# Optimization experiments

Hardware: AMD Instinct MI355X
Metric: run time of the kernel (lower is better)

## Reference

```python
import jax, jax.numpy as jnp
import numpy as np

N, E, D_IN, D_OUT, K = 50000, 800000, 128, 128, 3

def setup_inputs() -> dict:
    key = jax.random.key(0)
    k1, k2, k3, k4, k5 = jax.random.split(key, 5)
    feat = jax.random.normal(k1, (N, D_IN), dtype=jnp.float32)
    src = jax.random.randint(k2, (E,), 0, N)
    dst = jax.random.randint(k3, (E,), 0, N)
    theta = 0.1 * jax.random.normal(k4, (K + 1,), dtype=jnp.float32)
    # xavier-uniform-like linear weight [out, in]
    lim = float(np.sqrt(6.0 / (D_IN + D_OUT)))
    W = jax.random.uniform(k5, (D_OUT, D_IN), minval=-lim, maxval=lim, dtype=jnp.float32)
    return {"feat": feat, "src": src, "dst": dst, "theta": theta, "W": W}

def reference(feat, src, dst, theta, W):
    n = feat.shape[0]
    # in-degree per destination node, clamped to >= 1
    deg = jax.ops.segment_sum(jnp.ones_like(dst, dtype=feat.dtype), dst, num_segments=n)
    d_invsqrt = jnp.maximum(deg, 1.0) ** -0.5  # [N]
    d_invsqrt = d_invsqrt[:, None]

    def L_prime(x):
        # -D^{-1/2} A D^{-1/2} x  (A aggregates src -> dst)
        msg = (x * d_invsqrt)[src]                      # [E, D]
        agg = jax.ops.segment_sum(msg, dst, num_segments=n)
        return -agg * d_invsqrt

    k = theta.shape[0] - 1
    h = theta[0] * feat
    T_km2 = feat
    T_km1 = L_prime(feat)
    if k >= 1:
        h = h + theta[1] * (T_km1 + 1.0) * 0.5
    for order in range(2, k + 1):
        T_k = 2.0 * L_prime(T_km1) - T_km2
        h = h + theta[order] * (T_k + 1.0) * 0.5
        T_km2, T_km1 = T_km1, T_k

    out = h @ W.T  # linear, no bias
    return jax.nn.leaky_relu(out, negative_slope=0.01)
```

## Files before the change

### kernel.cpp

```cpp
#include <hip/hip_runtime.h>

#define NN 50000
#define EE 800000
#define D 128
#define PARTSZ 6250

static inline size_t align_up(size_t x, size_t a) { return (x + a - 1) & ~(a - 1); }

__device__ __forceinline__ unsigned pack_bf16(float a, float b) {
    unsigned ua = __float_as_uint(a), ub = __float_as_uint(b);
    unsigned ra = (ua + 0x7fffu + ((ua >> 16) & 1u)) >> 16;
    unsigned rb = (ub + 0x7fffu + ((ub >> 16) & 1u)) & 0xffff0000u;
    return ra | rb;
}
__device__ __forceinline__ float bf_lo(unsigned u) { return __uint_as_float(u << 16); }
__device__ __forceinline__ float bf_hi(unsigned u) { return __uint_as_float(u & 0xffff0000u); }

__global__ void zero_kernel(int* __restrict__ p, int n) {
    int i = blockIdx.x * blockDim.x + threadIdx.x;
    if (i < n) p[i] = 0;
}

__global__ __launch_bounds__(256) void deg_kernel(const int* __restrict__ dst,
                                                  int* __restrict__ deg, int E) {
    int part = blockIdx.x & 7;
    int nch = gridDim.x >> 3;
    int chunk = blockIdx.x >> 3;
    int per = (E + nch - 1) / nch;
    int beg = chunk * per;
    int end = min(E, beg + per);
    int plo = part * PARTSZ, phi = plo + PARTSZ;
    for (int e = beg + threadIdx.x; e < end; e += 256) {
        int d = dst[e];
        if (d >= plo && d < phi) atomicAdd(&deg[d], 1);
    }
}

__global__ void dinv_kernel(const int* __restrict__ deg, float* __restrict__ dinv,
                            float* __restrict__ rdinv, int n) {
    int i = blockIdx.x * blockDim.x + threadIdx.x;
    if (i < n) {
        float d = (float)deg[i];
        if (d < 1.0f) d = 1.0f;
        dinv[i] = rsqrtf(d);
        rdinv[i] = sqrtf(d);
    }
}

__global__ void scale_kernel(const float* __restrict__ feat, const float* __restrict__ dinv,
                             unsigned* __restrict__ featb, int n) {
    int idx = blockIdx.x * blockDim.x + threadIdx.x;
    if (idx >= n * 64) return;
    int i = idx >> 6;
    float di = dinv[i];
    float2 f = ((const float2*)feat)[idx];
    featb[idx] = pack_bf16(f.x * di, f.y * di);
}

__global__ void scan_blk_kernel(const int* __restrict__ deg, int* __restrict__ bscan,
                                int* __restrict__ btot, int n) {
    __shared__ int ws4[4];
    int tid = threadIdx.x, b = blockIdx.x;
    int i = b * 256 + tid;
    int v = (i < n) ? deg[i] : 0;
    int lane = tid & 63, w = tid >> 6;
    int sc = v;
    #pragma unroll
    for (int off = 1; off < 64; off <<= 1) {
        int t = __shfl_up(sc, off);
        if (lane >= off) sc += t;
    }
    if (lane == 63) ws4[w] = sc;
    __syncthreads();
    int woff = 0;
    #pragma unroll
    for (int k = 0; k < 4; ++k)
        if (k < w) woff += ws4[k];
    int inc = sc + woff;
    bscan[b * 256 + tid] = inc;
    if (tid == 255) btot[b] = inc;
}

__global__ void scan_top_kernel(int* __restrict__ btot, int nb) {
    __shared__ int ws4[4];
    int tid = threadIdx.x;
    int v = (tid < nb) ? btot[tid] : 0;
    int lane = tid & 63, w = tid >> 6;
    int sc = v;
    #pragma unroll
    for (int off = 1; off < 64; off <<= 1) {
        int t = __shfl_up(sc, off);
        if (lane >= off) sc += t;
    }
    if (lane == 63) ws4[w] = sc;
    __syncthreads();
    int woff = 0;
    #pragma unroll
    for (int k = 0; k < 4; ++k)
        if (k < w) woff += ws4[k];
    if (tid < nb) btot[tid] = sc + woff - v;
}

__global__ void scan_fix_kernel(const int* __restrict__ bscan, const int* __restrict__ btot,
                                const int* __restrict__ deg, int* __restrict__ rowptr,
                                int* __restrict__ cursor, int n) {
    int i = blockIdx.x * blockDim.x + threadIdx.x;
    if (i >= n) return;
    int inc = bscan[i] + btot[i >> 8];
    rowptr[i + 1] = inc;
    cursor[i] = inc - deg[i];
    if (i == 0) rowptr[0] = 0;
}

__global__ __launch_bounds__(256) void scatter_kernel(const int* __restrict__ src,
                                                      const int* __restrict__ dst,
                                                      int* __restrict__ cursor,
                                                      int* __restrict__ csr_src, int E) {
    int part = blockIdx.x & 7;
    int nch = gridDim.x >> 3;
    int chunk = blockIdx.x >> 3;
    int per = (E + nch - 1) / nch;
    int beg = chunk * per;
    int end = min(E, beg + per);
    int plo = part * PARTSZ, phi = plo + PARTSZ;
    for (int e = beg + threadIdx.x; e < end; e += 256) {
        int d = dst[e];
        if (d >= plo && d < phi) {
            int s = src[e];
            int p = atomicAdd(&cursor[d], 1);
            csr_src[p] = s;
        }
    }
}

#define ACC8(u) do { \
    a0 += bf_lo((u).x); a1 += bf_hi((u).x); \
    a2 += bf_lo((u).y); a3 += bf_hi((u).y); \
    a4 += bf_lo((u).z); a5 += bf_hi((u).z); \
    a6 += bf_lo((u).w); a7 += bf_hi((u).w); } while (0)

template <int MODE>
__global__ __launch_bounds__(256) void agg_kernel(
    const int* __restrict__ rowptr, const int* __restrict__ csr_src,
    const float* __restrict__ dinv, const float* __restrict__ rdinv,
    const unsigned* __restrict__ Xb, const unsigned* __restrict__ featb,
    const unsigned* __restrict__ T1b, const float* __restrict__ theta,
    unsigned* __restrict__ outb, int n) {
    int wid = (blockIdx.x * blockDim.x + threadIdx.x) >> 6;
    int lane = threadIdx.x & 63;
    if (wid >= n) return;
    int q = lane >> 4;
    int hq = lane & 15;
    int beg = rowptr[wid];
    int end = rowptr[wid + 1];
    const uint4* X4 = (const uint4*)Xb;
    float a0 = 0.f, a1 = 0.f, a2 = 0.f, a3 = 0.f, a4 = 0.f, a5 = 0.f, a6 = 0.f, a7 = 0.f;
    for (int e0 = beg; e0 < end; e0 += 64) {
        int s = (e0 + lane < end) ? csr_src[e0 + lane] : 0;
        int cnt = min(64, end - e0);
        int j = 0;
        for (; j + 16 <= cnt; j += 16) {
            int s0 = __shfl(s, j + q);
            int s1 = __shfl(s, j + 4 + q);
            int s2 = __shfl(s, j + 8 + q);
            int s3 = __shfl(s, j + 12 + q);
            uint4 u0 = X4[(size_t)s0 * 16 + hq];
            uint4 u1 = X4[(size_t)s1 * 16 + hq];
            uint4 u2 = X4[(size_t)s2 * 16 + hq];
            uint4 u3 = X4[(size_t)s3 * 16 + hq];
            ACC8(u0); ACC8(u1); ACC8(u2); ACC8(u3);
        }
        for (; j + 4 <= cnt; j += 4) {
            int s0 = __shfl(s, j + q);
            uint4 u0 = X4[(size_t)s0 * 16 + hq];
            ACC8(u0);
        }
        int rem = cnt - j;
        if (rem > 0) {
            int idx = j + q;
            if (idx >= cnt) idx = cnt - 1;
            int sj = __shfl(s, idx);
            if (q < rem) {
                uint4 u = X4[(size_t)sj * 16 + hq];
                ACC8(u);
            }
        }
    }
    a0 += __shfl_xor(a0, 16); a0 += __shfl_xor(a0, 32);
    a1 += __shfl_xor(a1, 16); a1 += __shfl_xor(a1, 32);
    a2 += __shfl_xor(a2, 16); a2 += __shfl_xor(a2, 32);
    a3 += __shfl_xor(a3, 16); a3 += __shfl_xor(a3, 32);
    a4 += __shfl_xor(a4, 16); a4 += __shfl_xor(a4, 32);
    a5 += __shfl_xor(a5, 16); a5 += __shfl_xor(a5, 32);
    a6 += __shfl_xor(a6, 16); a6 += __shfl_xor(a6, 32);
    a7 += __shfl_xor(a7, 16); a7 += __shfl_xor(a7, 32);

    if (q != 0) return;
    float di = dinv[wid];
    size_t r16 = (size_t)wid * 16 + hq;
    uint4 p;
    if (MODE == 1) {
        float m = -di * di;
        p.x = pack_bf16(m * a0, m * a1);
        p.y = pack_bf16(m * a2, m * a3);
        p.z = pack_bf16(m * a4, m * a5);
        p.w = pack_bf16(m * a6, m * a7);
    } else if (MODE == 2) {
        uint4 fb = ((const uint4*)featb)[r16];
        float m = -2.f * di * di;
        p.x = pack_bf16(m * a0 - bf_lo(fb.x), m * a1 - bf_hi(fb.x));
        p.y = pack_bf16(m * a2 - bf_lo(fb.y), m * a3 - bf_hi(fb.y));
        p.z = pack_bf16(m * a4 - bf_lo(fb.z), m * a5 - bf_hi(fb.z));
        p.w = pack_bf16(m * a6 - bf_lo(fb.w), m * a7 - bf_hi(fb.w));
    } else {
        uint4 fb = ((const uint4*)featb)[r16];
        uint4 b1 = ((const uint4*)T1b)[r16];
        uint4 b2 = ((const uint4*)Xb)[r16];
        float rd = rdinv[wid];
        float th0 = theta[0], th1 = theta[1], th2 = theta[2], th3 = theta[3];
        float c = 0.5f * (th1 + th2 + th3);
        float h[8];
        float av[8] = {a0, a1, a2, a3, a4, a5, a6, a7};
        float fv[8] = {bf_lo(fb.x), bf_hi(fb.x), bf_lo(fb.y), bf_hi(fb.y),
                       bf_lo(fb.z), bf_hi(fb.z), bf_lo(fb.w), bf_hi(fb.w)};
        float t1v[8] = {bf_lo(b1.x), bf_hi(b1.x), bf_lo(b1.y), bf_hi(b1.y),
                        bf_lo(b1.z), bf_hi(b1.z), bf_lo(b1.w), bf_hi(b1.w)};
        float t2v[8] = {bf_lo(b2.x), bf_hi(b2.x), bf_lo(b2.y), bf_hi(b2.y),
                        bf_lo(b2.z), bf_hi(b2.z), bf_lo(b2.w), bf_hi(b2.w)};
        #pragma unroll
        for (int k = 0; k < 8; ++k) {
            float t1 = t1v[k] * rd;
            float t2 = t2v[k] * rd;
            float f = fv[k] * rd;
            float t3 = -2.f * di * av[k] - t1;
            h[k] = th0 * f + 0.5f * (th1 * t1 + th2 * t2 + th3 * t3) + c;
        }
        p.x = pack_bf16(h[0], h[1]);
        p.y = pack_bf16(h[2], h[3]);
        p.z = pack_bf16(h[4], h[5]);
        p.w = pack_bf16(h[6], h[7]);
    }
    ((uint4*)outb)[r16] = p;
}

#define BK 32
#define TS 68
__global__ __launch_bounds__(256) void gemm_kernel(const unsigned* __restrict__ hb,
                                                   const float* __restrict__ W,
                                                   float* __restrict__ out, int n) {
    __shared__ float hs[BK * TS];
    __shared__ float ws[BK * TS];
    int tid = threadIdx.x;
    int tile = blockIdx.x >> 1;
    int o0 = (blockIdx.x & 1) * 64;
    int node0 = tile * 64;
    int tx = tid & 15, ty = tid >> 4;
    const uint2* H2 = (const uint2*)hb;

    float acc[4][4] = {};

    for (int k0 = 0; k0 < D; k0 += BK) {
        __syncthreads();
        #pragma unroll
        for (int p = 0; p < 2; ++p) {
            int idx = p * 256 + tid;
            int r = idx >> 3, c = idx & 7;
            int nn = node0 + r;
            uint2 u = make_uint2(0u, 0u);
            if (nn < n) u = H2[(size_t)nn * 32 + (k0 >> 2) + c];
            hs[(c * 4 + 0) * TS + r] = bf_lo(u.x);
            hs[(c * 4 + 1) * TS + r] = bf_hi(u.x);
            hs[(c * 4 + 2) * TS + r] = bf_lo(u.y);
            hs[(c * 4 + 3) * TS + r] = bf_hi(u.y);
            float4 wv = ((const float4*)(W + (size_t)(o0 + r) * D + k0))[c];
            ws[(c * 4 + 0) * TS + r] = wv.x;
            ws[(c * 4 + 1) * TS + r] = wv.y;
            ws[(c * 4 + 2) * TS + r] = wv.z;
            ws[(c * 4 + 3) * TS + r] = wv.w;
        }
        __syncthreads();
        #pragma unroll
        for (int kk = 0; kk < BK; ++kk) {
            float4 hv = *(const float4*)&hs[kk * TS + 4 * ty];
            float4 wv = *(const float4*)&ws[kk * TS + 4 * tx];
            float hvv[4] = {hv.x, hv.y, hv.z, hv.w};
            float wvv[4] = {wv.x, wv.y, wv.z, wv.w};
            #pragma unroll
            for (int k = 0; k < 4; ++k)
                #pragma unroll
                for (int kk2 = 0; kk2 < 4; ++kk2)
                    acc[k][kk2] = fmaf(hvv[k], wvv[kk2], acc[k][kk2]);
        }
    }

    #pragma unroll
    for (int k = 0; k < 4; ++k) {
        int nn = node0 + 4 * ty + k;
        if (nn < n) {
            float4 r4;
            r4.x = acc[k][0] > 0.f ? acc[k][0] : 0.01f * acc[k][0];
            r4.y = acc[k][1] > 0.f ? acc[k][1] : 0.01f * acc[k][1];
            r4.z = acc[k][2] > 0.f ? acc[k][2] : 0.01f * acc[k][2];
            r4.w = acc[k][3] > 0.f ? acc[k][3] : 0.01f * acc[k][3];
            ((float4*)(out + (size_t)nn * D + o0))[tx] = r4;
        }
    }
}

extern "C" void kernel_launch(void* const* d_in, const int* in_sizes, int n_in,
                              void* d_out, int out_size, void* d_ws, size_t ws_size,
                              hipStream_t stream) {
    const float* feat = (const float*)d_in[0];
    const int* src = (const int*)d_in[1];
    const int* dst = (const int*)d_in[2];
    const float* theta = (const float*)d_in[3];
    const float* W = (const float*)d_in[4];
    float* out = (float*)d_out;

    const int n = NN;
    const int E = EE;
    const int nb = (n + 255) / 256;

    char* w = (char*)d_ws;
    size_t off = 0;
    int* deg = (int*)(w + off); off = align_up(off + (size_t)n * 4, 512);
    float* dinv = (float*)(w + off); off = align_up(off + (size_t)n * 4, 512);
    float* rdinv = (float*)(w + off); off = align_up(off + (size_t)n * 4, 512);
    int* rowptr = (int*)(w + off); off = align_up(off + (size_t)(n + 1) * 4, 512);
    int* cursor = (int*)(w + off); off = align_up(off + (size_t)n * 4, 512);
    int* bscan = (int*)(w + off); off = align_up(off + (size_t)(nb * 256) * 4, 512);
    int* btot = (int*)(w + off); off = align_up(off + (size_t)256 * 4, 512);
    int* csr_src = (int*)(w + off); off = align_up(off + (size_t)E * 4, 512);
    unsigned* featb = (unsigned*)(w + off); off = align_up(off + (size_t)n * 64 * 4, 512);
    unsigned* T1b = (unsigned*)(w + off); off = align_up(off + (size_t)n * 64 * 4, 512);
    unsigned* T2b = (unsigned*)(w + off); off = align_up(off + (size_t)n * 64 * 4, 512);
    unsigned* hb = (unsigned*)(w + off); off = align_up(off + (size_t)n * 64 * 4, 512);
    (void)ws_size;

    zero_kernel<<<(n + 255) / 256, 256, 0, stream>>>(deg, n);
    deg_kernel<<<2048, 256, 0, stream>>>(dst, deg, E);
    dinv_kernel<<<(n + 255) / 256, 256, 0, stream>>>(deg, dinv, rdinv, n);
    scale_kernel<<<(n * 64 + 255) / 256, 256, 0, stream>>>(feat, dinv, featb, n);
    scan_blk_kernel<<<nb, 256, 0, stream>>>(deg, bscan, btot, n);
    scan_top_kernel<<<1, 256, 0, stream>>>(btot, nb);
    scan_fix_kernel<<<(n + 255) / 256, 256, 0, stream>>>(bscan, btot, deg, rowptr, cursor, n);
    scatter_kernel<<<2048, 256, 0, stream>>>(src, dst, cursor, csr_src, E);

    int agg_grid = (n + 3) / 4;
    agg_kernel<1><<<agg_grid, 256, 0, stream>>>(rowptr, csr_src, dinv, rdinv, featb, featb, T1b, theta, T1b, n);
    agg_kernel<2><<<agg_grid, 256, 0, stream>>>(rowptr, csr_src, dinv, rdinv, T1b, featb, T1b, theta, T2b, n);
    agg_kernel<3><<<agg_grid, 256, 0, stream>>>(rowptr, csr_src, dinv, rdinv, T2b, featb, T1b, theta, hb, n);

    int gemm_grid = ((n + 63) / 64) * 2;
    gemm_kernel<<<gemm_grid, 256, 0, stream>>>(hb, W, out, n);
}
```

Baseline: 220.0 us.

## Slice bf16 feature matrices into column-major 16-wide slabs for cache-local gathers

Stores the bf16 feature, T1, T2 and h matrices as eight column slices of 16 features, each slice laid out node-major. Each aggregation block now handles one slice for four nodes, so the gathered working set per slice is 1.6 MB and should fit in L2. Each wavefront lane loads 8 bytes per edge and covers 16 edges at a time. The cost is eight times more blocks, each re-reading rowptr and csr_src and doing more shuffle reductions, and the scale and GEMM kernels are changed to read and write the new layout.

```diff
diff --git a/kernel.cpp b/kernel.cpp
--- a/kernel.cpp
+++ b/kernel.cpp
@@ -48,13 +48,19 @@
 }
 
 __global__ void scale_kernel(const float* __restrict__ feat, const float* __restrict__ dinv,
-                             unsigned* __restrict__ featb, int n) {
+                             uint2* __restrict__ featb2, int n) {
     int idx = blockIdx.x * blockDim.x + threadIdx.x;
-    if (idx >= n * 64) return;
-    int i = idx >> 6;
+    if (idx >= n * 32) return;
+    int i = idx >> 5;
+    int c = idx & 31;
+    int s = c >> 2;
+    int c2 = c & 3;
     float di = dinv[i];
-    float2 f = ((const float2*)feat)[idx];
-    featb[idx] = pack_bf16(f.x * di, f.y * di);
+    float4 f = ((const float4*)feat)[(size_t)i * 32 + c];
+    uint2 p;
+    p.x = pack_bf16(f.x * di, f.y * di);
+    p.y = pack_bf16(f.z * di, f.w * di);
+    featb2[((size_t)s * n + i) * 4 + c2] = p;
 }
 
 __global__ void scan_blk_kernel(const int* __restrict__ deg, int* __restrict__ bscan,
@@ -133,102 +139,72 @@
     }
 }
 
-#define ACC8(u) do { \
-    a0 += bf_lo((u).x); a1 += bf_hi((u).x); \
-    a2 += bf_lo((u).y); a3 += bf_hi((u).y); \
-    a4 += bf_lo((u).z); a5 += bf_hi((u).z); \
-    a6 += bf_lo((u).w); a7 += bf_hi((u).w); } while (0)
-
 template <int MODE>
 __global__ __launch_bounds__(256) void agg_kernel(
     const int* __restrict__ rowptr, const int* __restrict__ csr_src,
     const float* __restrict__ dinv, const float* __restrict__ rdinv,
-    const unsigned* __restrict__ Xb, const unsigned* __restrict__ featb,
-    const unsigned* __restrict__ T1b, const float* __restrict__ theta,
-    unsigned* __restrict__ outb, int n) {
-    int wid = (blockIdx.x * blockDim.x + threadIdx.x) >> 6;
+    const uint2* __restrict__ Xb, const uint2* __restrict__ featb,
+    const uint2* __restrict__ T1b, const float* __restrict__ theta,
+    uint2* __restrict__ outb, int n) {
+    int slice = blockIdx.x & 7;
+    int wid = (blockIdx.x >> 3) * 4 + (threadIdx.x >> 6);
     int lane = threadIdx.x & 63;
     if (wid >= n) return;
-    int q = lane >> 4;
-    int hq = lane & 15;
+    int es = lane >> 2;
+    int cg = lane & 3;
     int beg = rowptr[wid];
     int end = rowptr[wid + 1];
-    const uint4* X4 = (const uint4*)Xb;
-    float a0 = 0.f, a1 = 0.f, a2 = 0.f, a3 = 0.f, a4 = 0.f, a5 = 0.f, a6 = 0.f, a7 = 0.f;
+    const uint2* X2 = Xb + (size_t)slice * n * 4;
+    float a0 = 0.f, a1 = 0.f, a2 = 0.f, a3 = 0.f;
     for (int e0 = beg; e0 < end; e0 += 64) {
         int s = (e0 + lane < end) ? csr_src[e0 + lane] : 0;
         int cnt = min(64, end - e0);
-        int j = 0;
-        for (; j + 16 <= cnt; j += 16) {
-            int s0 = __shfl(s, j + q);
-            int s1 = __shfl(s, j + 4 + q);
-            int s2 = __shfl(s, j + 8 + q);
-            int s3 = __shfl(s, j + 12 + q);
-            uint4 u0 = X4[(size_t)s0 * 16 + hq];
-            uint4 u1 = X4[(size_t)s1 * 16 + hq];
-            uint4 u2 = X4[(size_t)s2 * 16 + hq];
-            uint4 u3 = X4[(size_t)s3 * 16 + hq];
-            ACC8(u0); ACC8(u1); ACC8(u2); ACC8(u3);
-        }
-        for (; j + 4 <= cnt; j += 4) {
-            int s0 = __shfl(s, j + q);
-            uint4 u0 = X4[(size_t)s0 * 16 + hq];
-            ACC8(u0);
-        }
-        int rem = cnt - j;
-        if (rem > 0) {
-            int idx = j + q;
-            if (idx >= cnt) idx = cnt - 1;
-            int sj = __shfl(s, idx);
-            if (q < rem) {
-                uint4 u = X4[(size_t)sj * 16 + hq];
-                ACC8(u);
+        for (int j = 0; j < cnt; j += 16) {
+            int edge = j + es;
+            int sj = __shfl(s, edge < cnt ? edge : cnt - 1);
+            uint2 u = X2[(size_t)sj * 4 + cg];
+            if (edge < cnt) {
+                a0 += bf_lo(u.x); a1 += bf_hi(u.x);
+                a2 += bf_lo(u.y); a3 += bf_hi(u.y);
             }
         }
     }
-    a0 += __shfl_xor(a0, 16); a0 += __shfl_xor(a0, 32);
-    a1 += __shfl_xor(a1, 16); a1 += __shfl_xor(a1, 32);
-    a2 += __shfl_xor(a2, 16); a2 += __shfl_xor(a2, 32);
-    a3 += __shfl_xor(a3, 16); a3 += __shfl_xor(a3, 32);
-    a4 += __shfl_xor(a4, 16); a4 += __shfl_xor(a4, 32);
-    a5 += __shfl_xor(a5, 16); a5 += __shfl_xor(a5, 32);
-    a6 += __shfl_xor(a6, 16); a6 += __shfl_xor(a6, 32);
-    a7 += __shfl_xor(a7, 16); a7 += __shfl_xor(a7, 32);
-
-    if (q != 0) return;
+    a0 += __shfl_xor(a0, 4); a1 += __shfl_xor(a1, 4);
+    a2 += __shfl_xor(a2, 4); a3 += __shfl_xor(a3, 4);
+    a0 += __shfl_xor(a0, 8); a1 += __shfl_xor(a1, 8);
+    a2 += __shfl_xor(a2, 8); a3 += __shfl_xor(a3, 8);
+    a0 += __shfl_xor(a0, 16); a1 += __shfl_xor(a1, 16);
+    a2 += __shfl_xor(a2, 16); a3 += __shfl_xor(a3, 16);
+    a0 += __shfl_xor(a0, 32); a1 += __shfl_xor(a1, 32);
+    a2 += __shfl_xor(a2, 32); a3 += __shfl_xor(a3, 32);
+
+    if (es != 0) return;
     float di = dinv[wid];
-    size_t r16 = (size_t)wid * 16 + hq;
-    uint4 p;
+    size_t rr = ((size_t)slice * n + wid) * 4 + cg;
+    uint2 p;
     if (MODE == 1) {
         float m = -di * di;
         p.x = pack_bf16(m * a0, m * a1);
         p.y = pack_bf16(m * a2, m * a3);
-        p.z = pack_bf16(m * a4, m * a5);
-        p.w = pack_bf16(m * a6, m * a7);
     } else if (MODE == 2) {
-        uint4 fb = ((const uint4*)featb)[r16];
+        uint2 fb = featb[rr];
         float m = -2.f * di * di;
         p.x = pack_bf16(m * a0 - bf_lo(fb.x), m * a1 - bf_hi(fb.x));
         p.y = pack_bf16(m * a2 - bf_lo(fb.y), m * a3 - bf_hi(fb.y));
-        p.z = pack_bf16(m * a4 - bf_lo(fb.z), m * a5 - bf_hi(fb.z));
-        p.w = pack_bf16(m * a6 - bf_lo(fb.w), m * a7 - bf_hi(fb.w));
     } else {
-        uint4 fb = ((const uint4*)featb)[r16];
-        uint4 b1 = ((const uint4*)T1b)[r16];
-        uint4 b2 = ((const uint4*)Xb)[r16];
+        uint2 fb = featb[rr];
+        uint2 b1 = T1b[rr];
+        uint2 b2 = Xb[rr];
         float rd = rdinv[wid];
         float th0 = theta[0], th1 = theta[1], th2 = theta[2], th3 = theta[3];
         float c = 0.5f * (th1 + th2 + th3);
-        float h[8];
-        float av[8] = {a0, a1, a2, a3, a4, a5, a6, a7};
-        float fv[8] = {bf_lo(fb.x), bf_hi(fb.x), bf_lo(fb.y), bf_hi(fb.y),
-                       bf_lo(fb.z), bf_hi(fb.z), bf_lo(fb.w), bf_hi(fb.w)};
-        float t1v[8] = {bf_lo(b1.x), bf_hi(b1.x), bf_lo(b1.y), bf_hi(b1.y),
-                        bf_lo(b1.z), bf_hi(b1.z), bf_lo(b1.w), bf_hi(b1.w)};
-        float t2v[8] = {bf_lo(b2.x), bf_hi(b2.x), bf_lo(b2.y), bf_hi(b2.y),
-                        bf_lo(b2.z), bf_hi(b2.z), bf_lo(b2.w), bf_hi(b2.w)};
+        float av[4] = {a0, a1, a2, a3};
+        float fv[4] = {bf_lo(fb.x), bf_hi(fb.x), bf_lo(fb.y), bf_hi(fb.y)};
+        float t1v[4] = {bf_lo(b1.x), bf_hi(b1.x), bf_lo(b1.y), bf_hi(b1.y)};
+        float t2v[4] = {bf_lo(b2.x), bf_hi(b2.x), bf_lo(b2.y), bf_hi(b2.y)};
+        float h[4];
         #pragma unroll
-        for (int k = 0; k < 8; ++k) {
+        for (int k = 0; k < 4; ++k) {
             float t1 = t1v[k] * rd;
             float t2 = t2v[k] * rd;
             float f = fv[k] * rd;
@@ -237,15 +213,13 @@
         }
         p.x = pack_bf16(h[0], h[1]);
         p.y = pack_bf16(h[2], h[3]);
-        p.z = pack_bf16(h[4], h[5]);
-        p.w = pack_bf16(h[6], h[7]);
-    }
-    ((uint4*)outb)[r16] = p;
+    }
+    outb[rr] = p;
 }
 
 #define BK 32
 #define TS 68
-__global__ __launch_bounds__(256) void gemm_kernel(const unsigned* __restrict__ hb,
+__global__ __launch_bounds__(256) void gemm_kernel(const uint2* __restrict__ hb,
                                                    const float* __restrict__ W,
                                                    float* __restrict__ out, int n) {
     __shared__ float hs[BK * TS];
@@ -255,7 +229,6 @@
     int o0 = (blockIdx.x & 1) * 64;
     int node0 = tile * 64;
     int tx = tid & 15, ty = tid >> 4;
-    const uint2* H2 = (const uint2*)hb;
 
     float acc[4][4] = {};
 
@@ -266,8 +239,10 @@
             int idx = p * 256 + tid;
             int r = idx >> 3, c = idx & 7;
             int nn = node0 + r;
+            int s = (k0 >> 4) + (c >> 2);
+            int c2 = c & 3;
             uint2 u = make_uint2(0u, 0u);
-            if (nn < n) u = H2[(size_t)nn * 32 + (k0 >> 2) + c];
+            if (nn < n) u = hb[((size_t)s * n + nn) * 4 + c2];
             hs[(c * 4 + 0) * TS + r] = bf_lo(u.x);
             hs[(c * 4 + 1) * TS + r] = bf_hi(u.x);
             hs[(c * 4 + 2) * TS + r] = bf_lo(u.y);
@@ -331,22 +306,22 @@
     int* bscan = (int*)(w + off); off = align_up(off + (size_t)(nb * 256) * 4, 512);
     int* btot = (int*)(w + off); off = align_up(off + (size_t)256 * 4, 512);
     int* csr_src = (int*)(w + off); off = align_up(off + (size_t)E * 4, 512);
-    unsigned* featb = (unsigned*)(w + off); off = align_up(off + (size_t)n * 64 * 4, 512);
-    unsigned* T1b = (unsigned*)(w + off); off = align_up(off + (size_t)n * 64 * 4, 512);
-    unsigned* T2b = (unsigned*)(w + off); off = align_up(off + (size_t)n * 64 * 4, 512);
-    unsigned* hb = (unsigned*)(w + off); off = align_up(off + (size_t)n * 64 * 4, 512);
+    uint2* featb = (uint2*)(w + off); off = align_up(off + (size_t)n * 32 * 8, 512);
+    uint2* T1b = (uint2*)(w + off); off = align_up(off + (size_t)n * 32 * 8, 512);
+    uint2* T2b = (uint2*)(w + off); off = align_up(off + (size_t)n * 32 * 8, 512);
+    uint2* hb = (uint2*)(w + off); off = align_up(off + (size_t)n * 32 * 8, 512);
     (void)ws_size;
 
     zero_kernel<<<(n + 255) / 256, 256, 0, stream>>>(deg, n);
     deg_kernel<<<2048, 256, 0, stream>>>(dst, deg, E);
     dinv_kernel<<<(n + 255) / 256, 256, 0, stream>>>(deg, dinv, rdinv, n);
-    scale_kernel<<<(n * 64 + 255) / 256, 256, 0, stream>>>(feat, dinv, featb, n);
+    scale_kernel<<<(n * 32 + 255) / 256, 256, 0, stream>>>(feat, dinv, featb, n);
     scan_blk_kernel<<<nb, 256, 0, stream>>>(deg, bscan, btot, n);
     scan_top_kernel<<<1, 256, 0, stream>>>(btot, nb);
     scan_fix_kernel<<<(n + 255) / 256, 256, 0, stream>>>(bscan, btot, deg, rowptr, cursor, n);
     scatter_kernel<<<2048, 256, 0, stream>>>(src, dst, cursor, csr_src, E);
 
-    int agg_grid = (n + 3) / 4;
+    int agg_grid = ((n + 3) / 4) * 8;
     agg_kernel<1><<<agg_grid, 256, 0, stream>>>(rowptr, csr_src, dinv, rdinv, featb, featb, T1b, theta, T1b, n);
     agg_kernel<2><<<agg_grid, 256, 0, stream>>>(rowptr, csr_src, dinv, rdinv, T1b, featb, T1b, theta, T2b, n);
     agg_kernel<3><<<agg_grid, 256, 0, stream>>>(rowptr, csr_src, dinv, rdinv, T2b, featb, T1b, theta, hb, n);
```

Result: slower. 453.2 us (+106.0%).

## Map one node per quarter-wavefront in SpMM aggregation instead of one per wave

Applied to the files above, without the earlier changes.

The aggregation kernel now gives each 16-lane quarter of a wavefront its own destination node, so a wave handles four nodes instead of one. Each quarter loads its own 16 neighbor indices and gathers rows with per-lane masking, which removes the cross-quarter shuffle reduction and the q!=0 early exit. This is meant to cut wasted lanes and reduction overhead, given the average in-degree of about 16. The cost is load imbalance among the four nodes sharing a wave, since the wave loops until the highest-degree node finishes.

```diff
diff --git a/kernel.cpp b/kernel.cpp
--- a/kernel.cpp
+++ b/kernel.cpp
@@ -146,58 +146,42 @@
     const unsigned* __restrict__ Xb, const unsigned* __restrict__ featb,
     const unsigned* __restrict__ T1b, const float* __restrict__ theta,
     unsigned* __restrict__ outb, int n) {
-    int wid = (blockIdx.x * blockDim.x + threadIdx.x) >> 6;
     int lane = threadIdx.x & 63;
-    if (wid >= n) return;
     int q = lane >> 4;
     int hq = lane & 15;
-    int beg = rowptr[wid];
-    int end = rowptr[wid + 1];
+    int node = (blockIdx.x * 4 + (threadIdx.x >> 6)) * 4 + q;
+    bool valid = node < n;
+    int nclamp = valid ? node : 0;
+    int beg = rowptr[nclamp];
+    int cnt = valid ? (rowptr[nclamp + 1] - beg) : 0;
     const uint4* X4 = (const uint4*)Xb;
     float a0 = 0.f, a1 = 0.f, a2 = 0.f, a3 = 0.f, a4 = 0.f, a5 = 0.f, a6 = 0.f, a7 = 0.f;
-    for (int e0 = beg; e0 < end; e0 += 64) {
-        int s = (e0 + lane < end) ? csr_src[e0 + lane] : 0;
-        int cnt = min(64, end - e0);
-        int j = 0;
-        for (; j + 16 <= cnt; j += 16) {
-            int s0 = __shfl(s, j + q);
-            int s1 = __shfl(s, j + 4 + q);
-            int s2 = __shfl(s, j + 8 + q);
-            int s3 = __shfl(s, j + 12 + q);
+    int qb = q << 4;
+    for (int base = 0;; base += 16) {
+        int rem = cnt - base;
+        if (!__any(rem > 0)) break;
+        int s = 0;
+        if (hq < rem) s = csr_src[beg + base + hq];
+        #pragma unroll
+        for (int j = 0; j < 16; j += 4) {
+            if (!__any(j < rem)) break;
+            int s0 = __shfl(s, qb + j + 0);
+            int s1 = __shfl(s, qb + j + 1);
+            int s2 = __shfl(s, qb + j + 2);
+            int s3 = __shfl(s, qb + j + 3);
             uint4 u0 = X4[(size_t)s0 * 16 + hq];
             uint4 u1 = X4[(size_t)s1 * 16 + hq];
             uint4 u2 = X4[(size_t)s2 * 16 + hq];
             uint4 u3 = X4[(size_t)s3 * 16 + hq];
-            ACC8(u0); ACC8(u1); ACC8(u2); ACC8(u3);
-        }
-        for (; j + 4 <= cnt; j += 4) {
-            int s0 = __shfl(s, j + q);
-            uint4 u0 = X4[(size_t)s0 * 16 + hq];
-            ACC8(u0);
-        }
-        int rem = cnt - j;
-        if (rem > 0) {
-            int idx = j + q;
-            if (idx >= cnt) idx = cnt - 1;
-            int sj = __shfl(s, idx);
-            if (q < rem) {
-                uint4 u = X4[(size_t)sj * 16 + hq];
-                ACC8(u);
-            }
-        }
-    }
-    a0 += __shfl_xor(a0, 16); a0 += __shfl_xor(a0, 32);
-    a1 += __shfl_xor(a1, 16); a1 += __shfl_xor(a1, 32);
-    a2 += __shfl_xor(a2, 16); a2 += __shfl_xor(a2, 32);
-    a3 += __shfl_xor(a3, 16); a3 += __shfl_xor(a3, 32);
-    a4 += __shfl_xor(a4, 16); a4 += __shfl_xor(a4, 32);
-    a5 += __shfl_xor(a5, 16); a5 += __shfl_xor(a5, 32);
-    a6 += __shfl_xor(a6, 16); a6 += __shfl_xor(a6, 32);
-    a7 += __shfl_xor(a7, 16); a7 += __shfl_xor(a7, 32);
-
-    if (q != 0) return;
-    float di = dinv[wid];
-    size_t r16 = (size_t)wid * 16 + hq;
+            if (j + 0 < rem) ACC8(u0);
+            if (j + 1 < rem) ACC8(u1);
+            if (j + 2 < rem) ACC8(u2);
+            if (j + 3 < rem) ACC8(u3);
+        }
+    }
+    if (!valid) return;
+    float di = dinv[node];
+    size_t r16 = (size_t)node * 16 + hq;
     uint4 p;
     if (MODE == 1) {
         float m = -di * di;
@@ -216,10 +200,9 @@
         uint4 fb = ((const uint4*)featb)[r16];
         uint4 b1 = ((const uint4*)T1b)[r16];
         uint4 b2 = ((const uint4*)Xb)[r16];
-        float rd = rdinv[wid];
+        float rd = rdinv[node];
         float th0 = theta[0], th1 = theta[1], th2 = theta[2], th3 = theta[3];
         float c = 0.5f * (th1 + th2 + th3);
-        float h[8];
         float av[8] = {a0, a1, a2, a3, a4, a5, a6, a7};
         float fv[8] = {bf_lo(fb.x), bf_hi(fb.x), bf_lo(fb.y), bf_hi(fb.y),
                        bf_lo(fb.z), bf_hi(fb.z), bf_lo(fb.w), bf_hi(fb.w)};
@@ -227,6 +210,7 @@
                         bf_lo(b1.z), bf_hi(b1.z), bf_lo(b1.w), bf_hi(b1.w)};
         float t2v[8] = {bf_lo(b2.x), bf_hi(b2.x), bf_lo(b2.y), bf_hi(b2.y),
                         bf_lo(b2.z), bf_hi(b2.z), bf_lo(b2.w), bf_hi(b2.w)};
+        float h[8];
         #pragma unroll
         for (int k = 0; k < 8; ++k) {
             float t1 = t1v[k] * rd;
@@ -346,7 +330,7 @@
     scan_fix_kernel<<<(n + 255) / 256, 256, 0, stream>>>(bscan, btot, deg, rowptr, cursor, n);
     scatter_kernel<<<2048, 256, 0, stream>>>(src, dst, cursor, csr_src, E);
 
-    int agg_grid = (n + 3) / 4;
+    int agg_grid = (n + 15) / 16;
     agg_kernel<1><<<agg_grid, 256, 0, stream>>>(rowptr, csr_src, dinv, rdinv, featb, featb, T1b, theta, T1b, n);
     agg_kernel<2><<<agg_grid, 256, 0, stream>>>(rowptr, csr_src, dinv, rdinv, T1b, featb, T1b, theta, T2b, n);
     agg_kernel<3><<<agg_grid, 256, 0, stream>>>(rowptr, csr_src, dinv, rdinv, T2b, featb, T1b, theta, hb, n);
```

New measurement: 216.7 us. No clear change (-1.5%).
